# Performance work log

Hardware: AMD Instinct MI355X
Metric: run time of the kernel (lower is better)

## Reference

```python
import jax, jax.numpy as jnp
import numpy as np

# problem constants (from config / init_kwargs)
OBJ = 1024        # object_size
D = 256           # diffraction_size == probe_size (pad = 0)
P = 256           # probe_size
S = 8             # num_slices
B = 256           # batch of scan indices
NSCAN = 4096      # number of scan positions
PX = 0.1          # pixel_size (Angstrom)
LAM = 0.0197      # wavelength (Angstrom, ~300 kV)
CONV = 0.025      # convergence angle (rad)
DZ = 2.0          # slice thickness (Angstrom)


def _freq_grids():
    f = jnp.fft.fftfreq(D, d=PX).astype(jnp.float32)
    kx, ky = jnp.meshgrid(f, f, indexing='ij')
    return kx, ky


def _probe(defocus, Cs, astig_mag, astig_angle, aperture_smooth):
    kx, ky = _freq_grids()
    k = jnp.sqrt(kx ** 2 + ky ** 2)
    k_angle = jnp.arctan2(ky, kx)
    chi = (np.pi * LAM * defocus * k ** 2
           + 0.5 * np.pi * LAM ** 3 * (Cs * 1e6) * k ** 4
           + np.pi * LAM * astig_mag * k ** 2 * jnp.cos(2.0 * (k_angle - astig_angle)))
    k_max = CONV / LAM
    smooth = jnp.abs(aperture_smooth) + 0.01
    aperture = jax.nn.sigmoid((k_max - k) / (k_max * smooth))
    probe_k = aperture.astype(jnp.complex64) * jnp.exp(1j * chi.astype(jnp.complex64))
    probe_real = jnp.fft.ifftshift(jnp.fft.ifft2(probe_k))
    probe_real = probe_real / jnp.sqrt(jnp.sum(jnp.abs(probe_real) ** 2))
    # crop(P) with P == D and c == h is the identity slice [0:D, 0:D]
    return probe_real


def _propagator():
    kx, ky = _freq_grids()
    k2 = kx ** 2 + ky ** 2
    return jnp.exp(1j * (np.pi * LAM * DZ * k2).astype(jnp.complex64))


def setup_inputs() -> dict:
    key = jax.random.key(0)
    k1, k2, k3, k4 = jax.random.split(key, 4)
    slice_amp = jnp.ones((S, OBJ, OBJ), dtype=jnp.float32) \
        + 0.05 * jax.random.normal(k1, (S, OBJ, OBJ), dtype=jnp.float32)
    slice_phase = 0.1 * jax.random.normal(k2, (S, OBJ, OBJ), dtype=jnp.float32)
    scan_positions = jax.random.randint(k3, (NSCAN, 2), 0, OBJ - P, dtype=jnp.int32)
    indices = jax.random.randint(k4, (B,), 0, NSCAN, dtype=jnp.int32)
    return {
        'slice_amp': slice_amp,
        'slice_phase': slice_phase,
        'defocus': jnp.float32(50.0),
        'Cs': jnp.float32(0.5),
        'astig_mag': jnp.float32(10.0),
        'astig_angle': jnp.float32(0.0),
        'aperture_smooth': jnp.float32(0.1),
        'scan_positions': scan_positions,
        'indices': indices,
    }


def reference(slice_amp, slice_phase, defocus, Cs, astig_mag, astig_angle,
              aperture_smooth, scan_positions, indices):
    probe = _probe(defocus, Cs, astig_mag, astig_angle, aperture_smooth)  # [D,D] c64
    H = _propagator()                                                      # [D,D] c64
    pos = scan_positions[indices]                                          # [B,2] (y,x)

    def gather_patch(t, yx):
        return jax.lax.dynamic_slice(t, (yx[0], yx[1]), (P, P))

    wave = jnp.broadcast_to(probe[None, :, :], (B, P, P))  # [B,P,P] c64
    for s in range(S):  # small fixed slice recurrence
        t = slice_amp[s].astype(jnp.complex64) * jnp.exp(1j * slice_phase[s].astype(jnp.complex64))
        patches = jax.vmap(gather_patch, in_axes=(None, 0))(t, pos)  # [B,P,P]
        exit_wave = wave * patches                      # pad = 0 since P == D
        wave = jnp.fft.ifft2(jnp.fft.fft2(exit_wave) * H)
    psi = jnp.fft.fft2(wave)                            # [B,D,D] complex64
    return psi
```

## Files before the change

kernel.cpp:

```cpp
#include <hip/hip_runtime.h>
#include <hip/hip_fp16.h>
#include <math.h>

typedef unsigned short u16;
typedef unsigned int   u32;

__device__ __forceinline__ bool is_f64(const void* amp){
  u32 u = ((const u32*)amp)[1];
  return ((u >> 20) & 0xFFF) >= 0x3FB;
}
__device__ __forceinline__ bool is_i64(const void* spos){
  const u32* p = (const u32*)spos;
  return (p[1] | p[3] | p[5]) == 0;
}
__device__ __forceinline__ float ldf(const void* p, size_t i, bool f64){
  return f64 ? (float)((const double*)p)[i] : ((const float*)p)[i];
}
__device__ __forceinline__ double lds_scalar(const void* p, bool f64){
  return f64 ? ((const double*)p)[0] : (double)((const float*)p)[0];
}
__device__ __forceinline__ int ldi(const void* p, size_t i, bool i64){
  return i64 ? (int)((const long long*)p)[i] : ((const int*)p)[i];
}

__device__ __forceinline__ u16 f2bf(float f){
  u32 u = __float_as_uint(f);
  u32 r = 0x7fffu + ((u >> 16) & 1u);
  return (u16)((u + r) >> 16);
}
__device__ __forceinline__ void stout(void* p, size_t i, float2 v){
  ((u32*)p)[i] = (u32)f2bf(v.y) | ((u32)f2bf(v.x) << 16);
}

template<int H>
__device__ __forceinline__ float2 ld_state(const void* p, size_t i){
  if (H){
    __half2 h = ((const __half2*)p)[i];
    return __half22float2(h);
  }
  return ((const float2*)p)[i];
}
template<int H>
__device__ __forceinline__ void st_state(void* p, size_t i, float2 v){
  if (H) ((__half2*)p)[i] = __floats2half2_rn(v.x, v.y);
  else   ((float2*)p)[i] = v;
}

__device__ __forceinline__ float2 cadd(float2 a, float2 b){ return make_float2(a.x+b.x, a.y+b.y); }
__device__ __forceinline__ float2 csub(float2 a, float2 b){ return make_float2(a.x-b.x, a.y-b.y); }
__device__ __forceinline__ float2 cmul(float2 a, float2 b){ return make_float2(a.x*b.x - a.y*b.y, a.x*b.y + a.y*b.x); }
__device__ __forceinline__ float2 cscale(float2 a, float s){ return make_float2(a.x*s, a.y*s); }

template<int SGN>
__device__ __forceinline__ void fft4(float2& a, float2& b, float2& c, float2& d){
  float2 apc = cadd(a,c), amc = csub(a,c);
  float2 bpd = cadd(b,d), bmd = csub(b,d);
  float2 jb = (SGN < 0) ? make_float2(bmd.y, -bmd.x) : make_float2(-bmd.y, bmd.x);
  a = cadd(apc, bpd);
  b = cadd(amc, jb);
  c = csub(apc, bpd);
  d = csub(amc, jb);
}
template<int SGN>
__device__ __forceinline__ float2 twc(float2 z, float re, float im){
  float i2 = (SGN < 0) ? im : -im;
  return make_float2(z.x*re - z.y*i2, z.x*i2 + z.y*re);
}
template<int SGN>
__device__ __forceinline__ void fft16(float2 v[16]){
  float2 h[16];
#pragma unroll
  for (int n1=0;n1<4;n1++){
    float2 a=v[n1], b=v[n1+4], c=v[n1+8], d=v[n1+12];
    fft4<SGN>(a,b,c,d);
    h[n1*4+0]=a; h[n1*4+1]=b; h[n1*4+2]=c; h[n1*4+3]=d;
  }
  const float C1=0.92387953251f, S1=0.38268343236f, C2=0.70710678119f;
  h[5]  = twc<SGN>(h[5],  C1,-S1);
  h[6]  = twc<SGN>(h[6],  C2,-C2);
  h[7]  = twc<SGN>(h[7],  S1,-C1);
  h[9]  = twc<SGN>(h[9],  C2,-C2);
  h[10] = twc<SGN>(h[10], 0.f,-1.f);
  h[11] = twc<SGN>(h[11],-C2,-C2);
  h[13] = twc<SGN>(h[13], S1,-C1);
  h[14] = twc<SGN>(h[14],-C2,-C2);
  h[15] = twc<SGN>(h[15],-C1, S1);
#pragma unroll
  for (int q=0;q<4;q++){
    float2 a=h[q], b=h[4+q], c=h[8+q], d=h[12+q];
    fft4<SGN>(a,b,c,d);
    v[q]=a; v[q+4]=b; v[q+8]=c; v[q+12]=d;
  }
}

template<int SGN, int BARRIER>
__device__ __forceinline__ void fft256(float2 v[16], float* Tr, float* Ti, int g, int t){
  fft16<SGN>(v);
  float s0, c0;
  sincosf(0.0245436926f * (float)t, &s0, &c0);
  float2 w1 = make_float2(c0, (SGN < 0) ? -s0 : s0);
  float2 cw = w1;
#pragma unroll
  for (int q=1;q<16;q++){
    v[q] = cmul(v[q], cw);
    if (q < 15) cw = cmul(cw, w1);
  }
  int base = g*257;
  if (BARRIER) __syncthreads();
#pragma unroll
  for (int k1=0;k1<16;k1++){
    int o = base + t*16 + (k1^t);
    Tr[o] = v[k1].x; Ti[o] = v[k1].y;
  }
  if (BARRIER) __syncthreads();
#pragma unroll
  for (int n1=0;n1<16;n1++){
    int o = base + n1*16 + (t^n1);
    v[n1] = make_float2(Tr[o], Ti[o]);
  }
  fft16<SGN>(v);
  if (SGN > 0){
#pragma unroll
    for (int q=0;q<16;q++) v[q] = cscale(v[q], 1.f/256.f);
  }
}

__device__ __forceinline__ float ffreq(int i){ return (float)(i < 128 ? i : i - 256) * 0.0390625f; }

#define LDS_F 4112
#define KMAX  1.26903553299f
#define PHCONST 0.123778191f


__global__ void __launch_bounds__(256) probe_rowsF(const void* defocus, const void* Cs,
                                                   const void* astig_mag, const void* astig_angle,
                                                   const void* ap_smooth, const void* ampflag,
                                                   float2* tmp){
  __shared__ float Tr[LDS_F], Ti[LDS_F];
  bool f64 = is_f64(ampflag);
  int tid = threadIdx.x, g = tid>>4, t = tid&15;
  int r = blockIdx.x*16 + g;
  double df = lds_scalar(defocus, f64), cs = lds_scalar(Cs, f64);
  double am = lds_scalar(astig_mag, f64), aa = lds_scalar(astig_angle, f64);
  float sm = fabsf((float)lds_scalar(ap_smooth, f64)) + 0.01f;
  const double LAMd = 0.0197;
  float kxv = ffreq(r);
  float2 v[16];
#pragma unroll
  for (int j=0;j<16;j++){
    int c = t + 16*j;
    float kyv = ffreq(c);
    double k2 = (double)kxv*kxv + (double)kyv*kyv;
    float k  = sqrtf((float)k2);
    double ang = atan2((double)kyv, (double)kxv);
    double chi = M_PI*LAMd*df*k2
               + 0.5*M_PI*LAMd*LAMd*LAMd*(cs*1e6)*k2*k2
               + M_PI*LAMd*am*k2*cos(2.0*(ang - aa));
    float ap = 1.f/(1.f + expf(-(KMAX - k)/(KMAX*sm)));
    double sc = sin(chi), cc = cos(chi);
    v[j] = make_float2(ap*(float)cc, ap*(float)sc);
  }
  fft256<1,0>(v, Tr, Ti, g, t);
#pragma unroll
  for (int j=0;j<16;j++) tmp[(r<<8) + t + 16*j] = v[j];
}

__global__ void __launch_bounds__(256) probe_colsF(const float2* tmp, float2* probe_out,
                                                   const void* ap_smooth, const void* ampflag){
  __shared__ float Tr[LDS_F], Ti[LDS_F];
  bool f64 = is_f64(ampflag);
  int tid = threadIdx.x, xl = tid&15, t = tid>>4;
  int cx = blockIdx.x*16 + xl;
  float sm = fabsf((float)lds_scalar(ap_smooth, f64)) + 0.01f;
  float S = 0.f;
  for (int i = tid; i < 65536; i += 256){
    float kx = ffreq(i>>8), ky = ffreq(i&255);
    float k = sqrtf(kx*kx + ky*ky);
    float ap = 1.f/(1.f + expf(-(KMAX - k)/(KMAX*sm)));
    S += ap*ap;
  }
#pragma unroll
  for (int off=32; off>0; off>>=1) S += __shfl_down(S, off);
  if ((tid&63)==0) Tr[tid>>6] = S;
  __syncthreads();
  float scale = 256.f * rsqrtf(Tr[0]+Tr[1]+Tr[2]+Tr[3]);
  float2 v[16];
#pragma unroll
  for (int j=0;j<16;j++) v[j] = tmp[((t+16*j)<<8) + cx];
  fft256<1,1>(v, Tr, Ti, xl, t);
  int csh = (cx + 128) & 255;
#pragma unroll
  for (int j=0;j<16;j++){
    int y = t + 16*j;
    probe_out[(((y+128)&255)<<8) + csh] = cscale(v[j], scale);
  }
}

__global__ void __launch_bounds__(256) build_htabF(float2* htab){
  int tid = threadIdx.x;
#pragma unroll
  for (int k=0;k<4;k++){
    int i = blockIdx.x*1024 + tid + 256*k;
    float ky = ffreq(i>>8), kx = ffreq(i&255);
    float a = PHCONST*(kx*kx + ky*ky);
    float sa, ca; sincosf(a, &sa, &ca);
    htab[i] = make_float2(ca, sa);
  }
}

__global__ void __launch_bounds__(256) build_ttabF(const void* amp, const void* phase,
                                                   float2* ttab){
  bool f64 = is_f64(amp);
  int tid = threadIdx.x;
#pragma unroll
  for (int k=0;k<4;k++){
    size_t i = (size_t)blockIdx.x*1024 + tid + 256*k;
    float A = ldf(amp, i, f64);
    float P = ldf(phase, i, f64);
    float sp, cp; sincosf(P, &sp, &cp);
    ttab[i] = make_float2(A*cp, A*sp);
  }
}

template<int H>
__global__ void __launch_bounds__(256) row_passT(const void* amp, const void* phase,
                                                 const void* spos, const void* sidx,
                                                 void* state, const float2* probe,
                                                 const float2* ttab, int s, int first,
                                                 int use_tt){
  __shared__ float Tr[LDS_F], Ti[LDS_F];
  bool f64 = is_f64(amp);
  bool i64 = is_i64(spos);
  int tid = threadIdx.x, g = tid>>4, t = tid&15;
  int b = blockIdx.y;
  int y = blockIdx.x*16 + g;
  int n = ldi(sidx, b, i64);
  int py = ldi(spos, 2*(size_t)n, i64), px = ldi(spos, 2*(size_t)n+1, i64);
  size_t rowbase = ((size_t)s<<20) + (size_t)(py+y)*1024 + px;
  float2 tv[16];
  if (use_tt){
#pragma unroll
    for (int j=0;j<16;j++) tv[j] = ttab[rowbase + t + 16*j];
  } else {
#pragma unroll
    for (int j=0;j<16;j++){
      int x = t + 16*j;
      float A = ldf(amp,   rowbase + x, f64);
      float P = ldf(phase, rowbase + x, f64);
      float sp, cp; sincosf(P, &sp, &cp);
      tv[j] = make_float2(A*cp, A*sp);
    }
  }
  size_t ib = (size_t)b << 16;
  float2 v[16];
  if (first){
#pragma unroll
    for (int j=0;j<16;j++) v[j] = probe[(y<<8) + t + 16*j];
  } else {
#pragma unroll
    for (int j=0;j<16;j++) v[j] = ld_state<H>(state, ib + (y<<8) + t + 16*j);
    fft256<1,0>(v, Tr, Ti, g, t);
  }
#pragma unroll
  for (int j=0;j<16;j++) v[j] = cmul(v[j], tv[j]);
  fft256<-1,0>(v, Tr, Ti, g, t);
#pragma unroll
  for (int j=0;j<16;j++) st_state<H>(state, ib + (y<<8) + t + 16*j, v[j]);
}

template<int H>
__global__ void __launch_bounds__(256) col_passT(void* state, const float2* htab,
                                                 void* outp, int last){
  __shared__ float Tr[LDS_F], Ti[LDS_F];
  int tid = threadIdx.x, xl = tid&15, t = tid>>4;
  int b = blockIdx.y;
  int cx = blockIdx.x*16 + xl;
  size_t ib = (size_t)b << 16;
  float2 v[16], hv[16];
#pragma unroll
  for (int j=0;j<16;j++) v[j] = ld_state<H>(state, ib + ((t+16*j)<<8) + cx);
  if (!last){
#pragma unroll
    for (int j=0;j<16;j++) hv[j] = htab[((t+16*j)<<8) + cx];
  }
  fft256<-1,1>(v, Tr, Ti, xl, t);
  if (!last){
#pragma unroll
    for (int j=0;j<16;j++) v[j] = cmul(v[j], hv[j]);
    fft256<1,1>(v, Tr, Ti, xl, t);
#pragma unroll
    for (int j=0;j<16;j++) st_state<H>(state, ib + ((t+16*j)<<8) + cx, v[j]);
  } else {
#pragma unroll
    for (int j=0;j<16;j++) stout(outp, ib + ((t+16*j)<<8) + cx, v[j]);
  }
}

template<int H>
static void run_new(const void* amp, const void* phase,
                    const void* df, const void* cs, const void* am, const void* aa,
                    const void* sm, const void* spos, const void* sidx, int B,
                    void* state, float2* ttab, int use_tt,
                    void* dout, hipStream_t stream){
  char* dob = (char*)dout;
  float2* probe = (float2*)dob;
  float2* ptmp  = (float2*)(dob + 524288);
  float2* htab  = (float2*)(dob + 1048576);
  probe_rowsF<<<16, 256, 0, stream>>>(df, cs, am, aa, sm, amp, ptmp);
  probe_colsF<<<16, 256, 0, stream>>>(ptmp, probe, sm, amp);
  build_htabF<<<64, 256, 0, stream>>>(htab);
  if (use_tt) build_ttabF<<<8192, 256, 0, stream>>>(amp, phase, ttab);
  dim3 grid(16, B);
  row_passT<H><<<grid, 256, 0, stream>>>(amp, phase, spos, sidx, state, probe, ttab, 0, 1, use_tt);
  col_passT<H><<<grid, 256, 0, stream>>>(state, htab, dout, 0);
  for (int s = 1; s < 8; s++){
    row_passT<H><<<grid, 256, 0, stream>>>(amp, phase, spos, sidx, state, probe, ttab, s, 0, use_tt);
    col_passT<H><<<grid, 256, 0, stream>>>(state, htab, dout, 0);
  }
  col_passT<H><<<grid, 256, 0, stream>>>(state, htab, dout, 1);
}

extern "C" void kernel_launch(void* const* d_in, const int* in_sizes, int n_in,
                              void* d_out, int out_size, void* d_ws, size_t ws_size,
                              hipStream_t stream) {
  const void* amp   = d_in[0];
  const void* phase = d_in[1];
  const void* df    = d_in[2];
  const void* cs    = d_in[3];
  const void* am    = d_in[4];
  const void* aa    = d_in[5];
  const void* sm    = d_in[6];
  const void* spos  = d_in[7];
  const void* sidx  = d_in[8];
  int B = in_sizes[8];
  (void)out_size; (void)n_in;

  size_t stateH = (size_t)B * 65536 * 4;
  const size_t ttabB = (size_t)8 * 1024 * 1024 * 8;
  if (ws_size >= stateH + ttabB){
    void*   state = d_ws;
    float2* ttab  = (float2*)((char*)d_ws + stateH);
    run_new<1>(amp, phase, df, cs, am, aa, sm, spos, sidx, B,
               state, ttab, 1, d_out, stream);
  } else if (ws_size >= stateH){
    run_new<1>(amp, phase, df, cs, am, aa, sm, spos, sidx, B,
               d_ws, (float2*)d_ws, 0, d_out, stream);
  } else {
    run_new<1>(amp, phase, df, cs, am, aa, sm, spos, sidx, B,
               d_out, (float2*)d_out, 0, d_out, stream);
  }
}
```

Measured before the change: 904.7 us.

## Eliminate final column round trip and compute separable propagator in shared memory

The last slice's column pass now does the forward FFT, applies the propagator, and writes the output directly. This skips the inverse FFT plus the forward FFT that followed it, since fft(ifft(x)) is the identity, and drops one full launch over the batch state. The propagator is factored as a product of 1D phase terms built per block in LDS, replacing the global htab table and its loads. Per-thread FFT twiddles are precomputed once and reused across FFTs. The trade-off is extra complex multiplies per element and a small LDS table.

```diff
diff --git a/kernel.cpp b/kernel.cpp
--- a/kernel.cpp
+++ b/kernel.cpp
@@ -49,6 +49,7 @@
 __device__ __forceinline__ float2 cadd(float2 a, float2 b){ return make_float2(a.x+b.x, a.y+b.y); }
 __device__ __forceinline__ float2 csub(float2 a, float2 b){ return make_float2(a.x-b.x, a.y-b.y); }
 __device__ __forceinline__ float2 cmul(float2 a, float2 b){ return make_float2(a.x*b.x - a.y*b.y, a.x*b.y + a.y*b.x); }
+__device__ __forceinline__ float2 cmulc(float2 a, float2 b){ return make_float2(a.x*b.x + a.y*b.y, a.y*b.x - a.x*b.y); }
 __device__ __forceinline__ float2 cscale(float2 a, float s){ return make_float2(a.x*s, a.y*s); }
 
 template<int SGN>
@@ -93,17 +94,22 @@
   }
 }
 
-template<int SGN, int BARRIER>
-__device__ __forceinline__ void fft256(float2 v[16], float* Tr, float* Ti, int g, int t){
-  fft16<SGN>(v);
+__device__ __forceinline__ void make_tw(float2 tw[15], int t){
   float s0, c0;
   sincosf(0.0245436926f * (float)t, &s0, &c0);
-  float2 w1 = make_float2(c0, (SGN < 0) ? -s0 : s0);
-  float2 cw = w1;
+  float2 w1 = make_float2(c0, -s0);
+  tw[0] = w1;
+#pragma unroll
+  for (int q=1;q<15;q++) tw[q] = cmul(tw[q-1], w1);
+}
+
+template<int SGN, int BARRIER>
+__device__ __forceinline__ void fft256(float2 v[16], float* Tr, float* Ti, int g, int t,
+                                       const float2 tw[15]){
+  fft16<SGN>(v);
 #pragma unroll
   for (int q=1;q<16;q++){
-    v[q] = cmul(v[q], cw);
-    if (q < 15) cw = cmul(cw, w1);
+    v[q] = (SGN < 0) ? cmul(v[q], tw[q-1]) : cmulc(v[q], tw[q-1]);
   }
   int base = g*257;
   if (BARRIER) __syncthreads();
@@ -160,7 +166,8 @@
     double sc = sin(chi), cc = cos(chi);
     v[j] = make_float2(ap*(float)cc, ap*(float)sc);
   }
-  fft256<1,0>(v, Tr, Ti, g, t);
+  float2 tw[15]; make_tw(tw, t);
+  fft256<1,0>(v, Tr, Ti, g, t, tw);
 #pragma unroll
   for (int j=0;j<16;j++) tmp[(r<<8) + t + 16*j] = v[j];
 }
@@ -187,24 +194,13 @@
   float2 v[16];
 #pragma unroll
   for (int j=0;j<16;j++) v[j] = tmp[((t+16*j)<<8) + cx];
-  fft256<1,1>(v, Tr, Ti, xl, t);
+  float2 tw[15]; make_tw(tw, t);
+  fft256<1,1>(v, Tr, Ti, xl, t, tw);
   int csh = (cx + 128) & 255;
 #pragma unroll
   for (int j=0;j<16;j++){
     int y = t + 16*j;
     probe_out[(((y+128)&255)<<8) + csh] = cscale(v[j], scale);
-  }
-}
-
-__global__ void __launch_bounds__(256) build_htabF(float2* htab){
-  int tid = threadIdx.x;
-#pragma unroll
-  for (int k=0;k<4;k++){
-    int i = blockIdx.x*1024 + tid + 256*k;
-    float ky = ffreq(i>>8), kx = ffreq(i&255);
-    float a = PHCONST*(kx*kx + ky*ky);
-    float sa, ca; sincosf(a, &sa, &ca);
-    htab[i] = make_float2(ca, sa);
   }
 }
 
@@ -252,6 +248,7 @@
     }
   }
   size_t ib = (size_t)b << 16;
+  float2 tw[15]; make_tw(tw, t);
   float2 v[16];
   if (first){
 #pragma unroll
@@ -259,40 +256,66 @@
   } else {
 #pragma unroll
     for (int j=0;j<16;j++) v[j] = ld_state<H>(state, ib + (y<<8) + t + 16*j);
-    fft256<1,0>(v, Tr, Ti, g, t);
+    fft256<1,0>(v, Tr, Ti, g, t, tw);
   }
 #pragma unroll
   for (int j=0;j<16;j++) v[j] = cmul(v[j], tv[j]);
-  fft256<-1,0>(v, Tr, Ti, g, t);
+  fft256<-1,0>(v, Tr, Ti, g, t, tw);
 #pragma unroll
   for (int j=0;j<16;j++) st_state<H>(state, ib + (y<<8) + t + 16*j, v[j]);
 }
 
 template<int H>
-__global__ void __launch_bounds__(256) col_passT(void* state, const float2* htab,
-                                                 void* outp, int last){
-  __shared__ float Tr[LDS_F], Ti[LDS_F];
+__global__ void __launch_bounds__(256) col_passT(void* state){
+  __shared__ float Tr[LDS_F], Ti[LDS_F];
+  __shared__ float2 h1[256];
   int tid = threadIdx.x, xl = tid&15, t = tid>>4;
   int b = blockIdx.y;
   int cx = blockIdx.x*16 + xl;
   size_t ib = (size_t)b << 16;
-  float2 v[16], hv[16];
+  {
+    float kk = ffreq(tid);
+    float a = PHCONST * kk * kk;
+    float sa, ca; sincosf(a, &sa, &ca);
+    h1[tid] = make_float2(ca, sa);
+  }
+  float2 tw[15]; make_tw(tw, t);
+  float2 v[16];
 #pragma unroll
   for (int j=0;j<16;j++) v[j] = ld_state<H>(state, ib + ((t+16*j)<<8) + cx);
-  if (!last){
-#pragma unroll
-    for (int j=0;j<16;j++) hv[j] = htab[((t+16*j)<<8) + cx];
-  }
-  fft256<-1,1>(v, Tr, Ti, xl, t);
-  if (!last){
-#pragma unroll
-    for (int j=0;j<16;j++) v[j] = cmul(v[j], hv[j]);
-    fft256<1,1>(v, Tr, Ti, xl, t);
-#pragma unroll
-    for (int j=0;j<16;j++) st_state<H>(state, ib + ((t+16*j)<<8) + cx, v[j]);
-  } else {
-#pragma unroll
-    for (int j=0;j<16;j++) stout(outp, ib + ((t+16*j)<<8) + cx, v[j]);
+  fft256<-1,1>(v, Tr, Ti, xl, t, tw);
+  float2 hx = h1[cx & 255];
+#pragma unroll
+  for (int j=0;j<16;j++) v[j] = cmul(v[j], cmul(h1[t + 16*j], hx));
+  fft256<1,1>(v, Tr, Ti, xl, t, tw);
+#pragma unroll
+  for (int j=0;j<16;j++) st_state<H>(state, ib + ((t+16*j)<<8) + cx, v[j]);
+}
+
+template<int H>
+__global__ void __launch_bounds__(256) col_finT(void* state, void* outp){
+  __shared__ float Tr[LDS_F], Ti[LDS_F];
+  __shared__ float2 h1[256];
+  int tid = threadIdx.x, xl = tid&15, t = tid>>4;
+  int b = blockIdx.y;
+  int cx = blockIdx.x*16 + xl;
+  size_t ib = (size_t)b << 16;
+  {
+    float kk = ffreq(tid);
+    float a = PHCONST * kk * kk;
+    float sa, ca; sincosf(a, &sa, &ca);
+    h1[tid] = make_float2(ca, sa);
+  }
+  float2 tw[15]; make_tw(tw, t);
+  float2 v[16];
+#pragma unroll
+  for (int j=0;j<16;j++) v[j] = ld_state<H>(state, ib + ((t+16*j)<<8) + cx);
+  fft256<-1,1>(v, Tr, Ti, xl, t, tw);
+  float2 hx = h1[cx & 255];
+#pragma unroll
+  for (int j=0;j<16;j++){
+    float2 r = cmul(v[j], cmul(h1[t + 16*j], hx));
+    stout(outp, ib + ((t+16*j)<<8) + cx, r);
   }
 }
 
@@ -305,19 +328,18 @@
   char* dob = (char*)dout;
   float2* probe = (float2*)dob;
   float2* ptmp  = (float2*)(dob + 524288);
-  float2* htab  = (float2*)(dob + 1048576);
   probe_rowsF<<<16, 256, 0, stream>>>(df, cs, am, aa, sm, amp, ptmp);
   probe_colsF<<<16, 256, 0, stream>>>(ptmp, probe, sm, amp);
-  build_htabF<<<64, 256, 0, stream>>>(htab);
   if (use_tt) build_ttabF<<<8192, 256, 0, stream>>>(amp, phase, ttab);
   dim3 grid(16, B);
   row_passT<H><<<grid, 256, 0, stream>>>(amp, phase, spos, sidx, state, probe, ttab, 0, 1, use_tt);
-  col_passT<H><<<grid, 256, 0, stream>>>(state, htab, dout, 0);
-  for (int s = 1; s < 8; s++){
+  col_passT<H><<<grid, 256, 0, stream>>>(state);
+  for (int s = 1; s < 7; s++){
     row_passT<H><<<grid, 256, 0, stream>>>(amp, phase, spos, sidx, state, probe, ttab, s, 0, use_tt);
-    col_passT<H><<<grid, 256, 0, stream>>>(state, htab, dout, 0);
-  }
-  col_passT<H><<<grid, 256, 0, stream>>>(state, htab, dout, 1);
+    col_passT<H><<<grid, 256, 0, stream>>>(state);
+  }
+  row_passT<H><<<grid, 256, 0, stream>>>(amp, phase, spos, sidx, state, probe, ttab, 7, 0, use_tt);
+  col_finT<H><<<grid, 256, 0, stream>>>(state, dout);
 }
 
 extern "C" void kernel_launch(void* const* d_in, const int* in_sizes, int n_in,
```

After: 838.9 us. 1.08x faster.
